# Optimization experiments

Measured on AMD Instinct MI355X. Metric: run time of the kernel, lower is better.

## Reference

```python
import jax, jax.numpy as jnp
import numpy as np

B, E, LC, LE, D = 32, 8, 256, 512, 256   # batch, evi_num, claim_len, evidence_len, emb_dim
OUT, H = 128, 1                          # attention hidden dim, head_num
NEG = -1e18


def setup_inputs() -> dict:
    key = jax.random.key(0)
    ks = jax.random.split(key, 8)
    claim = jax.random.normal(ks[0], (B, E, LC, D), jnp.float32)
    evidence = jax.random.normal(ks[1], (B, E, LE, D), jnp.float32)
    claim_len_mask = jax.random.randint(ks[2], (B, E, 1, LC), 0, 2).astype(jnp.int32)
    evidence_len_mask = jax.random.randint(ks[3], (B, E, 1, LE), 0, 2).astype(jnp.int32)
    s2d = 1.0 / np.sqrt(2 * D)
    so = 1.0 / np.sqrt(OUT)
    W1 = jax.random.normal(ks[4], (2 * D, OUT), jnp.float32) * s2d  # torch W1.weight.T
    w2 = jax.random.normal(ks[5], (OUT, H), jnp.float32) * so
    W2 = jax.random.normal(ks[6], (2 * D, OUT), jnp.float32) * s2d
    w1 = jax.random.normal(ks[7], (OUT, H), jnp.float32) * so
    return {"claim": claim, "claim_len_mask": claim_len_mask,
            "evidence": evidence, "evidence_len_mask": evidence_len_mask,
            "W1": W1, "w2": w2, "W2": W2, "w1": w1}


def _pooled_attend(seq, seq_mask, pooled, W, w):
    # seq: (B,E,L,D), pooled: (B,E,1,D), W: (2D,OUT), w: (OUT,H)
    # cat([seq, pooled_expanded]) @ W  ==  seq @ W[:D] + pooled @ W[D:]  (broadcast)
    h = jnp.tanh(seq @ W[:D] + pooled @ W[D:])          # (B,E,L,OUT)
    att = h @ w                                          # (B,E,L,H)
    mask = jnp.swapaxes(seq_mask, -1, -2).astype(bool)   # (B,E,L,1), broadcast over H
    att = jnp.where(mask, att, NEG)
    scores = jax.nn.softmax(att, axis=-2)                # softmax over L
    out = jnp.einsum('belh,beld->behd', scores, seq)     # (B,E,H,D)
    return out.reshape(out.shape[0], out.shape[1], 1, -1)  # (B,E,1,H*D)


def reference(claim, claim_len_mask, evidence, evidence_len_mask, W1, w2, W2, w1):
    c_mean = jnp.mean(claim, axis=-2, keepdims=True)     # (B,E,1,D)
    e_hat = _pooled_attend(evidence, evidence_len_mask, c_mean, W1, w2)
    e_mean = jnp.mean(evidence, axis=-2, keepdims=True)  # (B,E,1,D)
    c_hat = _pooled_attend(claim, claim_len_mask, e_mean, W2, w1)
    return c_hat, e_hat
```

## Files before the change

kernel.cpp:

```cpp
#include <hip/hip_runtime.h>
#include <hip/hip_bf16.h>
#include <math.h>

#define BE   256
#define DIM  256
#define OUTD 128
#define LCL  256
#define LEV  512
#define NEGV -1e18f

typedef short  bf16x8  __attribute__((ext_vector_type(8)));
typedef float  floatx4 __attribute__((ext_vector_type(4)));

union BF1 { __hip_bfloat16 h; unsigned short u; };
union BF2 { __hip_bfloat162 h; unsigned int u; };

__device__ __forceinline__ float fast_tanh(float x) {
    float xc = fminf(fmaxf(x, -15.f), 15.f);
    float e = __expf(2.f * xc);
    return (e - 1.f) * __builtin_amdgcn_rcpf(e + 1.f);
}

__device__ __forceinline__ void gl_lds16(const float4* g, float4* l) {
    __builtin_amdgcn_global_load_lds(
        (const __attribute__((address_space(1))) unsigned int*)(const void*)g,
        (__attribute__((address_space(3))) unsigned int*)(void*)l,
        16, 0, 0);
}

__global__ __launch_bounds__(512) void k_meanbias(
    const float* __restrict__ claim, const float* __restrict__ evidence,
    const float* __restrict__ W1, const float* __restrict__ W2,
    float* __restrict__ bias_e, float* __restrict__ bias_c,
    unsigned short* __restrict__ WT1, unsigned short* __restrict__ WT2)
{
    const int bid = blockIdx.x;
    const int t = threadIdx.x;
    if (bid >= BE) {
        const int side = bid - BE;
        const float* W = side ? W2 : W1;
        unsigned short* WT = side ? WT2 : WT1;
        for (int i = t; i < OUTD * DIM; i += 512) {
            const int d = i & (DIM - 1);
            const int n = i >> 8;
            BF1 c; c.h = __float2bfloat16(W[(size_t)d * OUTD + n]);
            WT[n * DIM + d] = c.u;
        }
        return;
    }
    const int pair = bid;
    const int d4 = t & 63, rg = t >> 6;
    __shared__ float4 smc[8][64];
    __shared__ float4 sme[8][64];
    __shared__ float mc[DIM], me[DIM];
    __shared__ float sb[2][2][OUTD];

    const float4* c4 = (const float4*)(claim + (size_t)pair * LCL * DIM);
    const float4* e4 = (const float4*)(evidence + (size_t)pair * LEV * DIM);
    float4 ac = make_float4(0.f, 0.f, 0.f, 0.f);
    float4 ae = make_float4(0.f, 0.f, 0.f, 0.f);
#pragma unroll 8
    for (int r = rg; r < LCL; r += 8) {
        const float4 v = c4[r * 64 + d4];
        ac.x += v.x; ac.y += v.y; ac.z += v.z; ac.w += v.w;
    }
#pragma unroll 8
    for (int r = rg; r < LEV; r += 8) {
        const float4 v = e4[r * 64 + d4];
        ae.x += v.x; ae.y += v.y; ae.z += v.z; ae.w += v.w;
    }
    smc[rg][d4] = ac; sme[rg][d4] = ae;
    __syncthreads();
    if (t < 64) {
        float4 s = make_float4(0.f, 0.f, 0.f, 0.f);
#pragma unroll
        for (int j = 0; j < 8; ++j) {
            const float4 v = smc[j][t];
            s.x += v.x; s.y += v.y; s.z += v.z; s.w += v.w;
        }
        ((float4*)mc)[t] = make_float4(s.x * (1.f / LCL), s.y * (1.f / LCL),
                                       s.z * (1.f / LCL), s.w * (1.f / LCL));
    } else if (t < 128) {
        const int u = t - 64;
        float4 s = make_float4(0.f, 0.f, 0.f, 0.f);
#pragma unroll
        for (int j = 0; j < 8; ++j) {
            const float4 v = sme[j][u];
            s.x += v.x; s.y += v.y; s.z += v.z; s.w += v.w;
        }
        ((float4*)me)[u] = make_float4(s.x * (1.f / LEV), s.y * (1.f / LEV),
                                       s.z * (1.f / LEV), s.w * (1.f / LEV));
    }
    __syncthreads();
    const int side = t >> 8, o = t & 127, dh = (t >> 7) & 1;
    const float* W = side ? W2 : W1;
    const float* m = side ? me : mc;
    float s = 0.f;
#pragma unroll 8
    for (int i = 0; i < 128; ++i) {
        const int d = dh * 128 + i;
        s += m[d] * W[(size_t)(DIM + d) * OUTD + o];
    }
    sb[side][dh][o] = s;
    __syncthreads();
    if (t < 256) {
        const int sd = t >> 7, oo = t & 127;
        const float bv = sb[sd][0][oo] + sb[sd][1][oo];
        (sd ? bias_c : bias_e)[pair * OUTD + oo] = bv;
    }
}

__global__ __launch_bounds__(512, 1) void k_fused(
    const float* __restrict__ claim, const float* __restrict__ evidence,
    const unsigned short* __restrict__ WT1, const unsigned short* __restrict__ WT2,
    const float* __restrict__ w2v, const float* __restrict__ w1v,
    const float* __restrict__ bias_e, const float* __restrict__ bias_c,
    const int* __restrict__ emask, const int* __restrict__ cmask,
    float* __restrict__ out)
{
    constexpr int TR  = 64;
    constexpr int SR4 = 65;
    __shared__ float4 sA4[2][TR * SR4];
    __shared__ float sred[4][TR];

    const int bid = blockIdx.x;
    const bool is_ev = (bid & 1) == 0;
    const int pair = bid >> 1;
    const float* __restrict__ seq  = is_ev ? evidence : claim;
    const unsigned short* __restrict__ WT = is_ev ? WT1 : WT2;
    const float* __restrict__ wvec = is_ev ? w2v : w1v;
    const float* __restrict__ bias = is_ev ? bias_e : bias_c;
    const int*   __restrict__ mask = is_ev ? emask : cmask;
    float* __restrict__ outp       = is_ev ? out + (size_t)BE * DIM : out;
    const int L  = is_ev ? LEV : LCL;
    const int NT = L >> 6;

    const int t = threadIdx.x;
    const int lane = t & 63;
    const int wv = t >> 6;
    const int wrowf = wv >> 2;
    const int wcg = wv & 3;
    const int q = lane >> 4, c16 = lane & 15;
    const int arowb = wrowf * 32;

    float bc[2], wc[2];
#pragma unroll
    for (int ct = 0; ct < 2; ++ct) {
        const int col = wcg * 32 + ct * 16 + c16;
        bc[ct] = bias[pair * OUTD + col];
        wc[ct] = wvec[col];
    }

    bf16x8 breg[16];
#pragma unroll
    for (int ks = 0; ks < 8; ++ks)
#pragma unroll
        for (int ct = 0; ct < 2; ++ct)
            breg[ks * 2 + ct] = *(const bf16x8*)(
                WT + (size_t)(wcg * 32 + ct * 16 + c16) * DIM + ks * 32 + q * 8);

    const float4* sp4 = (const float4*)(seq + (size_t)pair * L * DIM);

    auto stage = [&](int buf, int tile) {
        const float4* base = sp4 + (size_t)tile * (TR * 64);
#pragma unroll
        for (int j = 0; j < 8; ++j) {
            const int row = wv * 8 + j;
            gl_lds16(base + row * 64 + lane, &sA4[buf][row * SR4]);
        }
    };

    stage(0, 0);
    int cur = 0;

    float4 Oac = make_float4(0.f, 0.f, 0.f, 0.f);
    float m_run = -INFINITY, l_run = 0.f;

    for (int tile = 0; tile < NT; ++tile) {
        asm volatile("s_waitcnt vmcnt(0) lgkmcnt(0)" ::: "memory");
        __builtin_amdgcn_s_barrier();
        if (tile + 1 < NT) stage(cur ^ 1, tile + 1);
        const int mk = mask[pair * L + tile * TR + lane];

        floatx4 acc[2][2];
        acc[0][0] = (floatx4){0.f, 0.f, 0.f, 0.f};
        acc[0][1] = (floatx4){0.f, 0.f, 0.f, 0.f};
        acc[1][0] = (floatx4){0.f, 0.f, 0.f, 0.f};
        acc[1][1] = (floatx4){0.f, 0.f, 0.f, 0.f};
#pragma unroll
        for (int ks = 0; ks < 8; ++ks) {
#pragma unroll
            for (int ra = 0; ra < 2; ++ra) {
                const float4 lo = sA4[cur][(arowb + ra * 16 + c16) * SR4 + ks * 8 + q * 2];
                const float4 hi = sA4[cur][(arowb + ra * 16 + c16) * SR4 + ks * 8 + q * 2 + 1];
                union { bf16x8 v; BF2 p[4]; } ua;
                ua.p[0].h = __float22bfloat162_rn(make_float2(lo.x, lo.y));
                ua.p[1].h = __float22bfloat162_rn(make_float2(lo.z, lo.w));
                ua.p[2].h = __float22bfloat162_rn(make_float2(hi.x, hi.y));
                ua.p[3].h = __float22bfloat162_rn(make_float2(hi.z, hi.w));
#pragma unroll
                for (int ct = 0; ct < 2; ++ct)
                    acc[ra][ct] = __builtin_amdgcn_mfma_f32_16x16x32_bf16(
                        ua.v, breg[ks * 2 + ct], acc[ra][ct], 0, 0, 0);
            }
        }

#pragma unroll
        for (int ra = 0; ra < 2; ++ra) {
#pragma unroll
            for (int reg = 0; reg < 4; ++reg) {
                float s = fast_tanh(acc[ra][0][reg] + bc[0]) * wc[0]
                        + fast_tanh(acc[ra][1][reg] + bc[1]) * wc[1];
#pragma unroll
                for (int off = 1; off < 16; off <<= 1) s += __shfl_xor(s, off, 64);
                if (c16 == 0)
                    sred[wcg][arowb + ra * 16 + q * 4 + reg] = s;
            }
        }
        asm volatile("s_waitcnt lgkmcnt(0)" ::: "memory");
        __builtin_amdgcn_s_barrier();

        float a = sred[0][lane] + sred[1][lane] + sred[2][lane] + sred[3][lane];
        a = mk ? a : NEGV;
        float mx = a;
#pragma unroll
        for (int off = 1; off < 64; off <<= 1) mx = fmaxf(mx, __shfl_xor(mx, off, 64));
        const float newm = fmaxf(m_run, mx);
        const float e = __expf(a - newm);
        float sm = e;
#pragma unroll
        for (int off = 1; off < 64; off <<= 1) sm += __shfl_xor(sm, off, 64);
        const float scale = __expf(m_run - newm);
        l_run = l_run * scale + sm;
        m_run = newm;
        Oac.x *= scale; Oac.y *= scale; Oac.z *= scale; Oac.w *= scale;

#pragma unroll
        for (int r = 0; r < 8; ++r) {
            const int rw = wv * 8 + r;
            const float pl = __shfl(e, rw, 64);
            const float4 v = sA4[cur][rw * SR4 + lane];
            Oac.x += pl * v.x; Oac.y += pl * v.y; Oac.z += pl * v.z; Oac.w += pl * v.w;
        }
        cur ^= 1;
    }

    __syncthreads();
    ((float4*)sA4)[t] = Oac;
    __syncthreads();
    if (t < 64) {
        float4 s = make_float4(0.f, 0.f, 0.f, 0.f);
#pragma unroll
        for (int j = 0; j < 8; ++j) {
            const float4 v = ((float4*)sA4)[j * 64 + t];
            s.x += v.x; s.y += v.y; s.z += v.z; s.w += v.w;
        }
        const float inv = 1.f / l_run;
        ((float4*)(outp + (size_t)pair * DIM))[t] =
            make_float4(s.x * inv, s.y * inv, s.z * inv, s.w * inv);
    }
}

extern "C" void kernel_launch(void* const* d_in, const int* in_sizes, int n_in,
                              void* d_out, int out_size, void* d_ws, size_t ws_size,
                              hipStream_t stream) {
    const float* claim    = (const float*)d_in[0];
    const int*   cmask    = (const int*)  d_in[1];
    const float* evidence = (const float*)d_in[2];
    const int*   emask    = (const int*)  d_in[3];
    const float* W1       = (const float*)d_in[4];
    const float* w2       = (const float*)d_in[5];
    const float* W2       = (const float*)d_in[6];
    const float* w1       = (const float*)d_in[7];
    float* out = (float*)d_out;

    float* ws = (float*)d_ws;
    float* bias_e = ws;
    float* bias_c = bias_e + BE * OUTD;
    unsigned short* WT1 = (unsigned short*)(bias_c + BE * OUTD);
    unsigned short* WT2 = WT1 + OUTD * DIM;

    k_meanbias<<<BE + 2, 512, 0, stream>>>(claim, evidence, W1, W2,
                                           bias_e, bias_c, WT1, WT2);
    k_fused<<<2 * BE, 512, 0, stream>>>(claim, evidence, WT1, WT2, w2, w1,
                                        bias_e, bias_c, emask, cmask, out);
}
```

Measured before the change: 370.3 us.

## Split sequence into per-block chunks with fixed softmax bound and combine kernel

Replaces the one-block-per-sequence loop with an online softmax by many small blocks. Each block handles one 32-row chunk and writes partial weighted sums and normaliser sums, and a new combine kernel reduces them. The running max is replaced by a fixed upper bound M = sum|w|, which holds because tanh is bounded, so no cross-chunk max or rescaling is needed. This targets low occupancy and the imbalance between sequence lengths, at the cost of writing partials and one extra launch. A fully masked row would now give a zero normaliser rather than uniform weights.

New measurement: 330.8 us. 10.7% less time.

```diff
diff --git a/kernel.cpp b/kernel.cpp
--- a/kernel.cpp
+++ b/kernel.cpp
@@ -7,7 +7,11 @@
 #define OUTD 128
 #define LCL  256
 #define LEV  512
-#define NEGV -1e18f
+
+#define NCH_EV 16
+#define NCH_CL 8
+#define NCHP   (NCH_EV + NCH_CL)
+#define NBLK   (BE * NCHP)
 
 typedef short  bf16x8  __attribute__((ext_vector_type(8)));
 typedef float  floatx4 __attribute__((ext_vector_type(4)));
@@ -31,11 +35,14 @@
 __global__ __launch_bounds__(512) void k_meanbias(
     const float* __restrict__ claim, const float* __restrict__ evidence,
     const float* __restrict__ W1, const float* __restrict__ W2,
+    const float* __restrict__ w2v, const float* __restrict__ w1v,
     float* __restrict__ bias_e, float* __restrict__ bias_c,
-    unsigned short* __restrict__ WT1, unsigned short* __restrict__ WT2)
+    unsigned short* __restrict__ WT1, unsigned short* __restrict__ WT2,
+    float* __restrict__ Mval)
 {
     const int bid = blockIdx.x;
     const int t = threadIdx.x;
+    __shared__ float msum[8];
     if (bid >= BE) {
         const int side = bid - BE;
         const float* W = side ? W2 : W1;
@@ -46,6 +53,15 @@
             BF1 c; c.h = __float2bfloat16(W[(size_t)d * OUTD + n]);
             WT[n * DIM + d] = c.u;
         }
+        const float* wv_ = side ? w1v : w2v;
+        float av = (t < OUTD) ? fabsf(wv_[t]) : 0.f;
+#pragma unroll
+        for (int off = 1; off < 64; off <<= 1) av += __shfl_xor(av, off, 64);
+        if ((t & 63) == 0) msum[t >> 6] = av;
+        __syncthreads();
+        if (t == 0)
+            Mval[side] = msum[0] + msum[1] + msum[2] + msum[3]
+                       + msum[4] + msum[5] + msum[6] + msum[7];
         return;
     }
     const int pair = bid;
@@ -110,139 +126,113 @@
     }
 }
 
-__global__ __launch_bounds__(512, 1) void k_fused(
+__global__ __launch_bounds__(256, 2) void k_main(
     const float* __restrict__ claim, const float* __restrict__ evidence,
     const unsigned short* __restrict__ WT1, const unsigned short* __restrict__ WT2,
     const float* __restrict__ w2v, const float* __restrict__ w1v,
     const float* __restrict__ bias_e, const float* __restrict__ bias_c,
     const int* __restrict__ emask, const int* __restrict__ cmask,
-    float* __restrict__ out)
+    const float* __restrict__ Mval,
+    float* __restrict__ O_part, float* __restrict__ l_part)
 {
-    constexpr int TR  = 64;
+    constexpr int TR  = 32;
     constexpr int SR4 = 65;
-    __shared__ float4 sA4[2][TR * SR4];
+    __shared__ float4 sA4[TR * SR4];
     __shared__ float sred[4][TR];
 
     const int bid = blockIdx.x;
-    const bool is_ev = (bid & 1) == 0;
-    const int pair = bid >> 1;
+    const int pair = bid / NCHP;
+    const int c = bid - pair * NCHP;
+    const bool is_ev = c < NCH_EV;
+    const int chunk = is_ev ? c : c - NCH_EV;
     const float* __restrict__ seq  = is_ev ? evidence : claim;
     const unsigned short* __restrict__ WT = is_ev ? WT1 : WT2;
     const float* __restrict__ wvec = is_ev ? w2v : w1v;
     const float* __restrict__ bias = is_ev ? bias_e : bias_c;
     const int*   __restrict__ mask = is_ev ? emask : cmask;
-    float* __restrict__ outp       = is_ev ? out + (size_t)BE * DIM : out;
-    const int L  = is_ev ? LEV : LCL;
-    const int NT = L >> 6;
+    const int L = is_ev ? LEV : LCL;
+    const float M = Mval[is_ev ? 0 : 1];
 
     const int t = threadIdx.x;
     const int lane = t & 63;
     const int wv = t >> 6;
-    const int wrowf = wv >> 2;
-    const int wcg = wv & 3;
     const int q = lane >> 4, c16 = lane & 15;
-    const int arowb = wrowf * 32;
 
     float bc[2], wc[2];
 #pragma unroll
     for (int ct = 0; ct < 2; ++ct) {
-        const int col = wcg * 32 + ct * 16 + c16;
+        const int col = wv * 32 + ct * 16 + c16;
         bc[ct] = bias[pair * OUTD + col];
         wc[ct] = wvec[col];
     }
-
     bf16x8 breg[16];
 #pragma unroll
     for (int ks = 0; ks < 8; ++ks)
 #pragma unroll
         for (int ct = 0; ct < 2; ++ct)
             breg[ks * 2 + ct] = *(const bf16x8*)(
-                WT + (size_t)(wcg * 32 + ct * 16 + c16) * DIM + ks * 32 + q * 8);
-
-    const float4* sp4 = (const float4*)(seq + (size_t)pair * L * DIM);
-
-    auto stage = [&](int buf, int tile) {
-        const float4* base = sp4 + (size_t)tile * (TR * 64);
-#pragma unroll
-        for (int j = 0; j < 8; ++j) {
-            const int row = wv * 8 + j;
-            gl_lds16(base + row * 64 + lane, &sA4[buf][row * SR4]);
-        }
-    };
-
-    stage(0, 0);
-    int cur = 0;
+                WT + (size_t)(wv * 32 + ct * 16 + c16) * DIM + ks * 32 + q * 8);
+
+    const float4* base = (const float4*)(seq + ((size_t)pair * L + chunk * TR) * DIM);
+#pragma unroll
+    for (int j = 0; j < 8; ++j) {
+        const int row = wv * 8 + j;
+        gl_lds16(base + row * 64 + lane, &sA4[row * SR4]);
+    }
+    const int mk = mask[pair * L + chunk * TR + (lane & 31)];
+    __syncthreads();
+
+    floatx4 acc[2][2];
+    acc[0][0] = (floatx4){0.f, 0.f, 0.f, 0.f};
+    acc[0][1] = (floatx4){0.f, 0.f, 0.f, 0.f};
+    acc[1][0] = (floatx4){0.f, 0.f, 0.f, 0.f};
+    acc[1][1] = (floatx4){0.f, 0.f, 0.f, 0.f};
+#pragma unroll
+    for (int ks = 0; ks < 8; ++ks) {
+#pragma unroll
+        for (int ra = 0; ra < 2; ++ra) {
+            const float4 lo = sA4[(ra * 16 + c16) * SR4 + ks * 8 + q * 2];
+            const float4 hi = sA4[(ra * 16 + c16) * SR4 + ks * 8 + q * 2 + 1];
+            union { bf16x8 v; BF2 p[4]; } ua;
+            ua.p[0].h = __float22bfloat162_rn(make_float2(lo.x, lo.y));
+            ua.p[1].h = __float22bfloat162_rn(make_float2(lo.z, lo.w));
+            ua.p[2].h = __float22bfloat162_rn(make_float2(hi.x, hi.y));
+            ua.p[3].h = __float22bfloat162_rn(make_float2(hi.z, hi.w));
+#pragma unroll
+            for (int ct = 0; ct < 2; ++ct)
+                acc[ra][ct] = __builtin_amdgcn_mfma_f32_16x16x32_bf16(
+                    ua.v, breg[ks * 2 + ct], acc[ra][ct], 0, 0, 0);
+        }
+    }
+
+#pragma unroll
+    for (int ra = 0; ra < 2; ++ra) {
+#pragma unroll
+        for (int reg = 0; reg < 4; ++reg) {
+            float s = fast_tanh(acc[ra][0][reg] + bc[0]) * wc[0]
+                    + fast_tanh(acc[ra][1][reg] + bc[1]) * wc[1];
+#pragma unroll
+            for (int off = 1; off < 16; off <<= 1) s += __shfl_xor(s, off, 64);
+            if (c16 == 0)
+                sred[wv][ra * 16 + q * 4 + reg] = s;
+        }
+    }
+    __syncthreads();
+
+    const int r31 = lane & 31;
+    const float a = sred[0][r31] + sred[1][r31] + sred[2][r31] + sred[3][r31];
+    const float e = mk ? __expf(a - M) : 0.f;
+    float sl = e;
+#pragma unroll
+    for (int off = 1; off < 32; off <<= 1) sl += __shfl_xor(sl, off, 64);
 
     float4 Oac = make_float4(0.f, 0.f, 0.f, 0.f);
-    float m_run = -INFINITY, l_run = 0.f;
-
-    for (int tile = 0; tile < NT; ++tile) {
-        asm volatile("s_waitcnt vmcnt(0) lgkmcnt(0)" ::: "memory");
-        __builtin_amdgcn_s_barrier();
-        if (tile + 1 < NT) stage(cur ^ 1, tile + 1);
-        const int mk = mask[pair * L + tile * TR + lane];
-
-        floatx4 acc[2][2];
-        acc[0][0] = (floatx4){0.f, 0.f, 0.f, 0.f};
-        acc[0][1] = (floatx4){0.f, 0.f, 0.f, 0.f};
-        acc[1][0] = (floatx4){0.f, 0.f, 0.f, 0.f};
-        acc[1][1] = (floatx4){0.f, 0.f, 0.f, 0.f};
-#pragma unroll
-        for (int ks = 0; ks < 8; ++ks) {
-#pragma unroll
-            for (int ra = 0; ra < 2; ++ra) {
-                const float4 lo = sA4[cur][(arowb + ra * 16 + c16) * SR4 + ks * 8 + q * 2];
-                const float4 hi = sA4[cur][(arowb + ra * 16 + c16) * SR4 + ks * 8 + q * 2 + 1];
-                union { bf16x8 v; BF2 p[4]; } ua;
-                ua.p[0].h = __float22bfloat162_rn(make_float2(lo.x, lo.y));
-                ua.p[1].h = __float22bfloat162_rn(make_float2(lo.z, lo.w));
-                ua.p[2].h = __float22bfloat162_rn(make_float2(hi.x, hi.y));
-                ua.p[3].h = __float22bfloat162_rn(make_float2(hi.z, hi.w));
-#pragma unroll
-                for (int ct = 0; ct < 2; ++ct)
-                    acc[ra][ct] = __builtin_amdgcn_mfma_f32_16x16x32_bf16(
-                        ua.v, breg[ks * 2 + ct], acc[ra][ct], 0, 0, 0);
-            }
-        }
-
-#pragma unroll
-        for (int ra = 0; ra < 2; ++ra) {
-#pragma unroll
-            for (int reg = 0; reg < 4; ++reg) {
-                float s = fast_tanh(acc[ra][0][reg] + bc[0]) * wc[0]
-                        + fast_tanh(acc[ra][1][reg] + bc[1]) * wc[1];
-#pragma unroll
-                for (int off = 1; off < 16; off <<= 1) s += __shfl_xor(s, off, 64);
-                if (c16 == 0)
-                    sred[wcg][arowb + ra * 16 + q * 4 + reg] = s;
-            }
-        }
-        asm volatile("s_waitcnt lgkmcnt(0)" ::: "memory");
-        __builtin_amdgcn_s_barrier();
-
-        float a = sred[0][lane] + sred[1][lane] + sred[2][lane] + sred[3][lane];
-        a = mk ? a : NEGV;
-        float mx = a;
-#pragma unroll
-        for (int off = 1; off < 64; off <<= 1) mx = fmaxf(mx, __shfl_xor(mx, off, 64));
-        const float newm = fmaxf(m_run, mx);
-        const float e = __expf(a - newm);
-        float sm = e;
-#pragma unroll
-        for (int off = 1; off < 64; off <<= 1) sm += __shfl_xor(sm, off, 64);
-        const float scale = __expf(m_run - newm);
-        l_run = l_run * scale + sm;
-        m_run = newm;
-        Oac.x *= scale; Oac.y *= scale; Oac.z *= scale; Oac.w *= scale;
-
-#pragma unroll
-        for (int r = 0; r < 8; ++r) {
-            const int rw = wv * 8 + r;
-            const float pl = __shfl(e, rw, 64);
-            const float4 v = sA4[cur][rw * SR4 + lane];
-            Oac.x += pl * v.x; Oac.y += pl * v.y; Oac.z += pl * v.z; Oac.w += pl * v.w;
-        }
-        cur ^= 1;
+#pragma unroll
+    for (int r = 0; r < 8; ++r) {
+        const int rw = wv * 8 + r;
+        const float pl = __shfl(e, rw, 64);
+        const float4 v = sA4[rw * SR4 + lane];
+        Oac.x += pl * v.x; Oac.y += pl * v.y; Oac.z += pl * v.z; Oac.w += pl * v.w;
     }
 
     __syncthreads();
@@ -251,14 +241,37 @@
     if (t < 64) {
         float4 s = make_float4(0.f, 0.f, 0.f, 0.f);
 #pragma unroll
-        for (int j = 0; j < 8; ++j) {
+        for (int j = 0; j < 4; ++j) {
             const float4 v = ((float4*)sA4)[j * 64 + t];
             s.x += v.x; s.y += v.y; s.z += v.z; s.w += v.w;
         }
-        const float inv = 1.f / l_run;
-        ((float4*)(outp + (size_t)pair * DIM))[t] =
-            make_float4(s.x * inv, s.y * inv, s.z * inv, s.w * inv);
-    }
+        ((float4*)(O_part + (size_t)bid * DIM))[t] = s;
+    }
+    if (t == 0) l_part[bid] = sl;
+}
+
+__global__ __launch_bounds__(64) void k_combine(
+    const float* __restrict__ O_part, const float* __restrict__ l_part,
+    float* __restrict__ out)
+{
+    const int bid = blockIdx.x;
+    const int t = threadIdx.x;
+    const bool is_ev = (bid & 1) == 0;
+    const int pair = bid >> 1;
+    const int base = pair * NCHP + (is_ev ? 0 : NCH_EV);
+    const int NC = is_ev ? NCH_EV : NCH_CL;
+    float* __restrict__ outp = is_ev ? out + (size_t)BE * DIM : out;
+
+    float4 s = make_float4(0.f, 0.f, 0.f, 0.f);
+    float l = 0.f;
+    for (int i = 0; i < NC; ++i) {
+        const float4 v = ((const float4*)(O_part + (size_t)(base + i) * DIM))[t];
+        s.x += v.x; s.y += v.y; s.z += v.z; s.w += v.w;
+        l += l_part[base + i];
+    }
+    const float inv = 1.f / l;
+    ((float4*)(outp + (size_t)pair * DIM))[t] =
+        make_float4(s.x * inv, s.y * inv, s.z * inv, s.w * inv);
 }
 
 extern "C" void kernel_launch(void* const* d_in, const int* in_sizes, int n_in,
@@ -277,11 +290,16 @@
     float* ws = (float*)d_ws;
     float* bias_e = ws;
     float* bias_c = bias_e + BE * OUTD;
-    unsigned short* WT1 = (unsigned short*)(bias_c + BE * OUTD);
+    float* O_part = bias_c + BE * OUTD;
+    float* l_part = O_part + (size_t)NBLK * DIM;
+    float* Mval   = l_part + NBLK;
+    unsigned short* WT1 = (unsigned short*)(Mval + 2);
     unsigned short* WT2 = WT1 + OUTD * DIM;
 
-    k_meanbias<<<BE + 2, 512, 0, stream>>>(claim, evidence, W1, W2,
-                                           bias_e, bias_c, WT1, WT2);
-    k_fused<<<2 * BE, 512, 0, stream>>>(claim, evidence, WT1, WT2, w2, w1,
-                                        bias_e, bias_c, emask, cmask, out);
-}
+    k_meanbias<<<BE + 2, 512, 0, stream>>>(claim, evidence, W1, W2, w2, w1,
+                                           bias_e, bias_c, WT1, WT2, Mval);
+    k_main<<<NBLK, 256, 0, stream>>>(claim, evidence, WT1, WT2, w2, w1,
+                                     bias_e, bias_c, emask, cmask, Mval,
+                                     O_part, l_part);
+    k_combine<<<2 * BE, 64, 0, stream>>>(O_part, l_part, out);
+}
```
